# Kernel tuning notes

Hardware: AMD Instinct MI355X
Metric: run time of the kernel (lower is better)

The kernel has to match this reference:

```python
import jax, jax.numpy as jnp
import numpy as np

D = 256      # d_model
A = 64       # attn_dim
K = 16       # k_neighbors
N = 20000    # embedding table rows
B = 32768    # batch of perturbed genes
SCALE = A ** -0.5
EPS = 1e-5


def setup_inputs() -> dict:
    key = jax.random.key(0)
    ks = jax.random.split(key, 12)
    all_embs = jax.random.normal(ks[0], (N, D), dtype=jnp.float32)
    center_idx = jax.random.randint(ks[1], (B,), 0, N)
    nb_idx = jax.random.randint(ks[2], (B, K), 0, N)
    nb_weights = jax.random.uniform(ks[3], (B, K), dtype=jnp.float32)
    # learned params (torch Linear weight layout: [out, in])
    s = lambda fan_in: 1.0 / np.sqrt(fan_in)
    Wq = jax.random.uniform(ks[4], (A, D), minval=-s(D), maxval=s(D))
    Wk = jax.random.uniform(ks[5], (A, D), minval=-s(D), maxval=s(D))
    Wg = jax.random.uniform(ks[6], (D, D), minval=-s(D), maxval=s(D))
    bg = jax.random.uniform(ks[7], (D,), minval=-s(D), maxval=s(D))
    Wo = jax.random.uniform(ks[8], (D, 2 * D), minval=-s(2 * D), maxval=s(2 * D))
    bo = jax.random.uniform(ks[9], (D,), minval=-s(2 * D), maxval=s(2 * D))
    gamma = jnp.ones((D,), jnp.float32)
    beta = jnp.zeros((D,), jnp.float32)
    return dict(all_embs=all_embs, center_idx=center_idx, nb_idx=nb_idx,
                nb_weights=nb_weights, Wq=Wq, Wk=Wk, Wg=Wg, bg=bg,
                Wo=Wo, bo=bo, gamma=gamma, beta=beta)


def reference(all_embs, center_idx, nb_idx, nb_weights, Wq, Wk, Wg, bg, Wo, bo, gamma, beta):
    center = all_embs[center_idx]                      # [B, D]
    nbs = all_embs[nb_idx]                             # [B, K, D]
    q = center @ Wq.T                                  # [B, A]
    k = jnp.einsum('bkd,ad->bka', nbs, Wk)             # [B, K, A]
    logits = jnp.einsum('ba,bka->bk', q, k) * SCALE
    logits = logits + jnp.log(jnp.clip(nb_weights, 1e-6))
    attn = jax.nn.softmax(logits, axis=-1)             # [B, K]
    gate = jax.nn.sigmoid(center @ Wg.T + bg)          # [B, D]
    context = gate * jnp.einsum('bk,bkd->bd', attn, nbs)
    combined = jnp.concatenate([center, context], axis=-1)  # [B, 2D]
    enriched = combined @ Wo.T + bo                    # [B, D]
    x = enriched + center
    mu = jnp.mean(x, axis=-1, keepdims=True)
    var = jnp.var(x, axis=-1, keepdims=True)
    return (x - mu) * jax.lax.rsqrt(var + EPS) * gamma + beta
```

## Files before the change

kernel.cpp:

```cpp
#include <hip/hip_runtime.h>

#define DD 256
#define MM 32

typedef __attribute__((ext_vector_type(8))) short bfrag;
typedef __attribute__((ext_vector_type(4))) float ffrag;
typedef __attribute__((ext_vector_type(2))) float f32x2;

__device__ __forceinline__ float lo2f(unsigned int p){ union{unsigned int i; float f;} v; v.i = p<<16; return v.f; }
__device__ __forceinline__ float hi2f(unsigned int p){ union{unsigned int i; float f;} v; v.i = p & 0xffff0000u; return v.f; }
__device__ __forceinline__ float bf2f(unsigned short u){ union{unsigned int i; float f;} v; v.i = ((unsigned int)u)<<16; return v.f; }
__device__ __forceinline__ unsigned short f2b(float x){
    union{float f; unsigned int i;} v; v.f = x;
    unsigned int r = v.i + 0x7fffu + ((v.i>>16)&1u);
    return (unsigned short)(r>>16);
}
__device__ __forceinline__ unsigned int pack2(float a, float b){
    return (unsigned int)f2b(a) | ((unsigned int)f2b(b)<<16);
}
__device__ __forceinline__ f32x2 up2(unsigned int p){
    f32x2 r; r.x = lo2f(p); r.y = hi2f(p); return r;
}

__device__ __forceinline__ int swz256(int d, int e){
    return ((d>>4)*8 + (e>>5))*512 + (((e>>3)&3)*16 + (d&15))*8 + (e&7);
}
__device__ __forceinline__ int swz512(int d, int e){
    return ((d>>4)*16 + (e>>5))*512 + (((e>>3)&3)*16 + (d&15))*8 + (e&7);
}

extern "C" __global__ __launch_bounds__(256)
void prep_all(const float* __restrict__ Wq, const float* __restrict__ Wk,
              const float* __restrict__ Wg, const float* __restrict__ Wo,
              const float* __restrict__ embs, unsigned short* __restrict__ ws, int n8)
{
    int bid = blockIdx.x, e = threadIdx.x;
    if (bid < 256) {
        int d = bid; float acc = 0.f;
        #pragma unroll 8
        for (int a = 0; a < 64; ++a) acc = fmaf(Wq[a*256 + e], Wk[a*256 + d], acc);
        ws[swz256(d, e)] = f2b(acc);
    } else if (bid < 512) {
        int r = bid - 256;
        ws[65536 + swz256(r, e)] = f2b(Wg[r*256 + e]);
    } else if (bid < 768) {
        int r = bid - 512;
        ws[131072 + swz512(r, e)]       = f2b(Wo[r*512 + e]);
        ws[131072 + swz512(r, e + 256)] = f2b(Wo[r*512 + 256 + e]);
    } else {
        int i = (bid - 768)*256 + e;
        if (i < n8) {
            const float4* s = (const float4*)embs + (size_t)i*2;
            float4 a = s[0], b = s[1];
            uint4 o;
            o.x = pack2(a.x,a.y); o.y = pack2(a.z,a.w);
            o.z = pack2(b.x,b.y); o.w = pack2(b.z,b.w);
            ((uint4*)(ws + 262144))[i] = o;
        }
    }
}

template<bool TBF>
__device__ __forceinline__ void gather8(uint4* buf, const unsigned short* tbl,
                                        const float* embs, int idx, int p)
{
    if (TBF) {
        const unsigned short* base = tbl + (size_t)idx*DD + p*8;
        #pragma unroll
        for (int i = 0; i < 8; ++i) buf[i] = *(const uint4*)(base + i*32);
    } else {
        const float* base = embs + (size_t)idx*DD + p*8;
        #pragma unroll
        for (int i = 0; i < 8; ++i) {
            float4 a = *(const float4*)(base + i*32);
            float4 b = *(const float4*)(base + i*32 + 4);
            buf[i].x = pack2(a.x,a.y); buf[i].y = pack2(a.z,a.w);
            buf[i].z = pack2(b.x,b.y); buf[i].w = pack2(b.z,b.w);
        }
    }
}

template<bool TBF>
__global__ __launch_bounds__(256, 2)
void na_mfma14(const float* __restrict__ embs,
               const int* __restrict__ cidx,
               const int* __restrict__ nidx,
               const float* __restrict__ nbw,
               const unsigned short* __restrict__ tbl,
               const unsigned short* __restrict__ wMt,
               const unsigned short* __restrict__ wWg,
               const unsigned short* __restrict__ wWo,
               const float* __restrict__ bg,
               const float* __restrict__ bo,
               const float* __restrict__ gamma,
               const float* __restrict__ beta,
               float* __restrict__ out)
{
    __shared__ __align__(16) unsigned short s_ax[32][264];
    __shared__ __align__(16) unsigned short s_arena[21120];
    __shared__ int s_cidx[32];

    unsigned short (*s_t)[264]      = (unsigned short(*)[264])s_arena;
    unsigned short (*s_nb)[16][264] = (unsigned short(*)[16][264])(s_arena + 4224);
    float* s_x = (float*)s_arena;

    const int tid  = threadIdx.x;
    const int row0 = blockIdx.x * MM;
    const int lane = tid & 63, wv = tid >> 6;
    const int l15  = lane & 15, quad = lane >> 4;
    const ffrag fz = {0.f, 0.f, 0.f, 0.f};

    if (tid < 32) s_cidx[tid] = cidx[row0 + tid];
    uint4 careg0[8], careg1[8];
    {
        int a0 = cidx[row0 + l15];
        int a1 = cidx[row0 + 16 + l15];
        if (TBF) {
            const unsigned short* p0 = tbl + (size_t)a0*DD + quad*8;
            const unsigned short* p1 = tbl + (size_t)a1*DD + quad*8;
            #pragma unroll
            for (int kc = 0; kc < 8; ++kc) {
                careg0[kc] = *(const uint4*)(p0 + kc*32);
                careg1[kc] = *(const uint4*)(p1 + kc*32);
            }
        } else {
            const float* p0 = embs + (size_t)a0*DD + quad*8;
            const float* p1 = embs + (size_t)a1*DD + quad*8;
            #pragma unroll
            for (int kc = 0; kc < 8; ++kc) {
                float4 a = *(const float4*)(p0 + kc*32);
                float4 b = *(const float4*)(p0 + kc*32 + 4);
                careg0[kc].x = pack2(a.x,a.y); careg0[kc].y = pack2(a.z,a.w);
                careg0[kc].z = pack2(b.x,b.y); careg0[kc].w = pack2(b.z,b.w);
                float4 c = *(const float4*)(p1 + kc*32);
                float4 d = *(const float4*)(p1 + kc*32 + 4);
                careg1[kc].x = pack2(c.x,c.y); careg1[kc].y = pack2(c.z,c.w);
                careg1[kc].z = pack2(d.x,d.y); careg1[kc].w = pack2(d.z,d.w);
            }
        }
    }

    ffrag at1[4] = {fz,fz,fz,fz};
    {
        ffrag at0[4] = {fz,fz,fz,fz};
        ffrag ag0[4] = {fz,fz,fz,fz}, ag1[4] = {fz,fz,fz,fz};
        const unsigned short* btA = wMt + (size_t)(wv*4)*4096 + lane*8;
        const unsigned short* bgA = wWg + (size_t)(wv*4)*4096 + lane*8;
        #pragma unroll
        for (int kc = 0; kc < 8; ++kc) {
            bfrag a0 = *(const bfrag*)&careg0[kc];
            bfrag a1 = *(const bfrag*)&careg1[kc];
            #pragma unroll
            for (int t = 0; t < 4; ++t) {
                bfrag bm = *(const bfrag*)(btA + (size_t)t*4096 + kc*512);
                at0[t] = __builtin_amdgcn_mfma_f32_16x16x32_bf16(a0, bm, at0[t], 0,0,0);
                at1[t] = __builtin_amdgcn_mfma_f32_16x16x32_bf16(a1, bm, at1[t], 0,0,0);
                bfrag bw = *(const bfrag*)(bgA + (size_t)t*4096 + kc*512);
                ag0[t] = __builtin_amdgcn_mfma_f32_16x16x32_bf16(a0, bw, ag0[t], 0,0,0);
                ag1[t] = __builtin_amdgcn_mfma_f32_16x16x32_bf16(a1, bw, ag1[t], 0,0,0);
            }
        }
        #pragma unroll
        for (int t = 0; t < 4; ++t) {
            int col = wv*64 + t*16 + l15;
            float bgv = bg[col];
            #pragma unroll
            for (int r = 0; r < 4; ++r) {
                int rr = quad*4 + r;
                s_t[rr][col] = f2b(at0[t][r]);
                float g0 = 1.f / (1.f + __expf(-(ag0[t][r] + bgv)));
                s_ax[rr][col] = f2b(g0);
                float g1 = 1.f / (1.f + __expf(-(ag1[t][r] + bgv)));
                s_ax[16 + rr][col] = f2b(g1);
            }
        }
    }
    __syncthreads();

    const int kn = lane >> 2;
    const int p  = lane & 3;
    auto attn_phase = [&](int rb) {
        int idxs[4];
        #pragma unroll
        for (int j = 0; j < 4; ++j)
            idxs[j] = nidx[(size_t)(row0 + rb + 4*wv + j) * 16 + kn];

        uint4 buf[2][8];
        gather8<TBF>(buf[0], tbl, embs, idxs[0], p);

        #pragma unroll
        for (int j = 0; j < 4; ++j) {
            if (j < 3) gather8<TBF>(buf[(j+1)&1], tbl, embs, idxs[j+1], p);
            const int ml = 4*wv + j;
            const int mg = rb + ml;
            unsigned short* nbp = &s_nb[wv][kn][p*8];
            #pragma unroll
            for (int i = 0; i < 8; ++i) *(uint4*)(nbp + i*32) = buf[j&1][i];
            const unsigned short* trow = &s_t[ml][p*8];
            f32x2 part2 = {0.f, 0.f};
            #pragma unroll
            for (int i = 0; i < 8; ++i) {
                uint4 v = buf[j&1][i];
                uint4 tv = *(const uint4*)(trow + i*32);
                part2 += up2(v.x) * up2(tv.x);
                part2 += up2(v.y) * up2(tv.y);
                part2 += up2(v.z) * up2(tv.z);
                part2 += up2(v.w) * up2(tv.w);
            }
            float part = part2.x + part2.y;
            part += __shfl_xor(part, 1);
            part += __shfl_xor(part, 2);
            float lg = part * 0.125f;
            float mx = lg;
            mx = fmaxf(mx, __shfl_xor(mx, 4));  mx = fmaxf(mx, __shfl_xor(mx, 8));
            mx = fmaxf(mx, __shfl_xor(mx, 16)); mx = fmaxf(mx, __shfl_xor(mx, 32));
            float wgt = fmaxf(nbw[(size_t)(row0 + mg) * 16 + kn], 1e-6f);
            float e = wgt * __expf(lg - mx);
            float s = e;
            s += __shfl_xor(s, 4);  s += __shfl_xor(s, 8);
            s += __shfl_xor(s, 16); s += __shfl_xor(s, 32);
            float attn = e / s;
            f32x2 c01 = {0.f, 0.f}, c23 = {0.f, 0.f};
            #pragma unroll
            for (int kk = 0; kk < 16; ++kk) {
                float a = __shfl(attn, kk*4);
                f32x2 a2; a2.x = a; a2.y = a;
                uint2 v = *(const uint2*)&s_nb[wv][kk][lane*4];
                c01 += a2 * up2(v.x);
                c23 += a2 * up2(v.y);
            }
            uint2 g = *(const uint2*)&s_ax[mg][lane*4];
            f32x2 g01 = up2(g.x), g23 = up2(g.y);
            c01 *= g01; c23 *= g23;
            uint2 o; o.x = pack2(c01.x, c01.y); o.y = pack2(c23.x, c23.y);
            *(uint2*)&s_ax[mg][lane*4] = o;
        }
    };

    attn_phase(0);
    __syncthreads();
    {
        #pragma unroll
        for (int t = 0; t < 4; ++t) {
            int col = wv*64 + t*16 + l15;
            #pragma unroll
            for (int r = 0; r < 4; ++r)
                s_t[quad*4 + r][col] = f2b(at1[t][r]);
        }
    }
    __syncthreads();
    attn_phase(16);
    __syncthreads();

    {
        ffrag acc0[4] = {fz,fz,fz,fz}, acc1[4] = {fz,fz,fz,fz};
        const unsigned short* arx0 = &s_ax[l15][quad * 8];
        const unsigned short* arx1 = &s_ax[16 + l15][quad * 8];
        const unsigned short* bO   = wWo + (size_t)(wv*4)*8192 + lane*8;
        #pragma unroll
        for (int kc = 0; kc < 8; ++kc) {
            bfrag a0 = *(const bfrag*)&careg0[kc];
            bfrag a1 = *(const bfrag*)&careg1[kc];
            #pragma unroll
            for (int t = 0; t < 4; ++t) {
                bfrag b = *(const bfrag*)(bO + (size_t)t*8192 + kc*512);
                acc0[t] = __builtin_amdgcn_mfma_f32_16x16x32_bf16(a0, b, acc0[t], 0,0,0);
                acc1[t] = __builtin_amdgcn_mfma_f32_16x16x32_bf16(a1, b, acc1[t], 0,0,0);
            }
        }
        #pragma unroll
        for (int kc = 8; kc < 16; ++kc) {
            bfrag a0 = *(const bfrag*)(arx0 + (kc-8)*32);
            bfrag a1 = *(const bfrag*)(arx1 + (kc-8)*32);
            #pragma unroll
            for (int t = 0; t < 4; ++t) {
                bfrag b = *(const bfrag*)(bO + (size_t)t*8192 + kc*512);
                acc0[t] = __builtin_amdgcn_mfma_f32_16x16x32_bf16(a0, b, acc0[t], 0,0,0);
                acc1[t] = __builtin_amdgcn_mfma_f32_16x16x32_bf16(a1, b, acc1[t], 0,0,0);
            }
        }
        #pragma unroll
        for (int t = 0; t < 4; ++t) {
            int col = wv*64 + t*16 + l15;
            float bov = bo[col];
            #pragma unroll
            for (int r = 0; r < 4; ++r) {
                int rr = quad*4 + r;
                float c0 = embs[(size_t)s_cidx[rr] * DD + col];
                s_x[rr*260 + col] = acc0[t][r] + bov + c0;
                float c1 = embs[(size_t)s_cidx[16 + rr] * DD + col];
                s_x[(16 + rr)*260 + col] = acc1[t][r] + bov + c1;
            }
        }
    }
    __syncthreads();

    {
        #pragma unroll
        for (int jj = 0; jj < 8; ++jj) {
            int m = wv * 8 + jj;
            const float* xr = s_x + m*260;
            float x0 = xr[lane],       x1 = xr[64 + lane];
            float x2 = xr[128 + lane], x3 = xr[192 + lane];
            float s  = x0 + x1 + x2 + x3;
            float ss = x0*x0 + x1*x1 + x2*x2 + x3*x3;
            #pragma unroll
            for (int off = 32; off >= 1; off >>= 1) {
                s  += __shfl_xor(s, off);
                ss += __shfl_xor(ss, off);
            }
            float mu  = s * (1.f/256.f);
            float var = ss * (1.f/256.f) - mu*mu;
            float rs  = rsqrtf(var + 1e-5f);
            size_t base = (size_t)(row0 + m) * DD;
            float xs[4] = {x0, x1, x2, x3};
            #pragma unroll
            for (int cc = 0; cc < 4; ++cc) {
                int dd = cc*64 + lane;
                out[base + dd] = (xs[cc] - mu) * rs * gamma[dd] + beta[dd];
            }
        }
    }
}

#define SD 260
#define KT 16
#define WS 17
#define FM 16
extern "C" __global__ __launch_bounds__(256)
void na_f32_kernel(const float* __restrict__ embs, const int* __restrict__ center_idx,
                   const int* __restrict__ nb_idx, const float* __restrict__ nb_w,
                   const float* __restrict__ Wq, const float* __restrict__ Wk,
                   const float* __restrict__ Wg, const float* __restrict__ bg,
                   const float* __restrict__ Wo, const float* __restrict__ bo,
                   const float* __restrict__ gamma, const float* __restrict__ beta,
                   float* __restrict__ out)
{
    __shared__ __align__(16) float s_center[FM][SD];
    __shared__ __align__(16) float s_tc[FM][SD];
    __shared__ __align__(16) float s_nb[16][SD];
    __shared__ __align__(16) float s_w[DD][WS];
    __shared__ __align__(16) float s_q[FM][64];
    __shared__ float s_red[16][16];
    __shared__ float s_attn[16];
    const int tid = threadIdx.x;
    const int row0 = blockIdx.x * FM;
    const int td = tid & 63, tm = tid >> 6;
    {
        int m = tid >> 4, c = tid & 15;
        int idx = center_idx[row0 + m];
        const float4* src = (const float4*)(embs + (size_t)idx * DD) + c * 4;
        float4* dst = (float4*)&s_center[m][c * 16];
        dst[0]=src[0]; dst[1]=src[1]; dst[2]=src[2]; dst[3]=src[3];
    }
    __syncthreads();
    {
        const int a = tid & 63, mg = tid >> 6;
        float qacc[4] = {0,0,0,0};
        for (int kt = 0; kt < DD; kt += KT) {
            __syncthreads();
            { int r = tid >> 2, c4 = (tid & 3) * 4;
              *(float4*)&s_w[r][c4] = *(const float4*)(Wq + r * DD + kt + c4); }
            __syncthreads();
            #pragma unroll
            for (int kk = 0; kk < KT; kk += 4) {
                float4 b = *(const float4*)&s_w[a][kk];
                #pragma unroll
                for (int i = 0; i < 4; ++i) {
                    float4 av = *(const float4*)&s_center[4*mg + i][kt + kk];
                    qacc[i] += av.x*b.x + av.y*b.y + av.z*b.z + av.w*b.w;
                }
            }
        }
        __syncthreads();
        #pragma unroll
        for (int i = 0; i < 4; ++i) s_q[4*mg + i][a] = qacc[i];
    }
    __syncthreads();
    {
        float tacc[4][4];
        #pragma unroll
        for (int i=0;i<4;++i) { tacc[i][0]=tacc[i][1]=tacc[i][2]=tacc[i][3]=0.f; }
        for (int kk = 0; kk < 64; kk += 4) {
            float4 bk[4];
            #pragma unroll
            for (int t4 = 0; t4 < 4; ++t4)
                bk[t4] = *(const float4*)(Wk + (size_t)(kk + t4) * DD + 4 * td);
            #pragma unroll
            for (int i = 0; i < 4; ++i) {
                float4 av = *(const float4*)&s_q[4*tm + i][kk];
                tacc[i][0] += av.x*bk[0].x + av.y*bk[1].x + av.z*bk[2].x + av.w*bk[3].x;
                tacc[i][1] += av.x*bk[0].y + av.y*bk[1].y + av.z*bk[2].y + av.w*bk[3].y;
                tacc[i][2] += av.x*bk[0].z + av.y*bk[1].z + av.z*bk[2].z + av.w*bk[3].z;
                tacc[i][3] += av.x*bk[0].w + av.y*bk[1].w + av.z*bk[2].w + av.w*bk[3].w;
            }
        }
        #pragma unroll
        for (int i = 0; i < 4; ++i)
            *(float4*)&s_tc[4*tm + i][4*td] = make_float4(tacc[i][0],tacc[i][1],tacc[i][2],tacc[i][3]);
    }
    __syncthreads();
    for (int m = 0; m < FM; ++m) {
        { int k = tid >> 4, c = tid & 15;
          int idx = nb_idx[(row0 + m) * 16 + k];
          const float4* src = (const float4*)(embs + (size_t)idx * DD) + c * 4;
          float4* dst = (float4*)&s_nb[k][c * 16];
          dst[0]=src[0]; dst[1]=src[1]; dst[2]=src[2]; dst[3]=src[3]; }
        __syncthreads();
        { int k = tid >> 4, i = tid & 15;
          float acc = 0.f;
          #pragma unroll
          for (int j4 = 0; j4 < 4; ++j4) {
              float4 nv = *(const float4*)&s_nb[k][i*16 + 4*j4];
              float4 tv = *(const float4*)&s_tc[m][i*16 + 4*j4];
              acc += nv.x*tv.x + nv.y*tv.y + nv.z*tv.z + nv.w*tv.w;
          }
          s_red[k][i] = acc; }
        __syncthreads();
        if (tid < 16) {
            float lg = 0.f;
            #pragma unroll
            for (int i = 0; i < 16; ++i) lg += s_red[tid][i];
            float wv2 = nb_w[(row0 + m) * 16 + tid];
            lg = lg * 0.125f + logf(fmaxf(wv2, 1e-6f));
            float mx = lg;
            #pragma unroll
            for (int off = 8; off >= 1; off >>= 1) mx = fmaxf(mx, __shfl_xor(mx, off));
            float e = expf(lg - mx);
            float s = e;
            #pragma unroll
            for (int off = 8; off >= 1; off >>= 1) s += __shfl_xor(s, off);
            s_attn[tid] = e / s;
        }
        __syncthreads();
        { float acc = 0.f;
          #pragma unroll
          for (int k = 0; k < 16; ++k) acc += s_attn[k] * s_nb[k][tid];
          s_tc[m][tid] = acc; }
        __syncthreads();
    }
    {
        float acc[4][4];
        #pragma unroll
        for (int i=0;i<4;++i){acc[i][0]=acc[i][1]=acc[i][2]=acc[i][3]=0.f;}
        for (int kt = 0; kt < DD; kt += KT) {
            __syncthreads();
            #pragma unroll
            for (int j = 0; j < 4; ++j) {
                int r = (tid >> 2) + 64 * j, c4 = (tid & 3) * 4;
                *(float4*)&s_w[r][c4] = *(const float4*)(Wg + (size_t)r * DD + kt + c4);
            }
            __syncthreads();
            #pragma unroll
            for (int kk = 0; kk < KT; kk += 4) {
                float4 b[4];
                #pragma unroll
                for (int j = 0; j < 4; ++j) b[j] = *(const float4*)&s_w[4*td + j][kk];
                #pragma unroll
                for (int i = 0; i < 4; ++i) {
                    float4 av = *(const float4*)&s_center[4*tm + i][kt + kk];
                    #pragma unroll
                    for (int j = 0; j < 4; ++j)
                        acc[i][j] += av.x*b[j].x + av.y*b[j].y + av.z*b[j].z + av.w*b[j].w;
                }
            }
        }
        float bgv[4];
        #pragma unroll
        for (int j = 0; j < 4; ++j) bgv[j] = bg[4*td + j];
        __syncthreads();
        #pragma unroll
        for (int i = 0; i < 4; ++i)
            #pragma unroll
            for (int j = 0; j < 4; ++j) {
                float g = 1.f / (1.f + expf(-(acc[i][j] + bgv[j])));
                s_tc[4*tm + i][4*td + j] *= g;
            }
    }
    {
        float acc[4][4];
        #pragma unroll
        for (int i=0;i<4;++i){acc[i][0]=acc[i][1]=acc[i][2]=acc[i][3]=0.f;}
        for (int kt = 0; kt < 2*DD; kt += KT) {
            __syncthreads();
            #pragma unroll
            for (int j = 0; j < 4; ++j) {
                int r = (tid >> 2) + 64 * j, c4 = (tid & 3) * 4;
                *(float4*)&s_w[r][c4] = *(const float4*)(Wo + (size_t)r * 2 * DD + kt + c4);
            }
            __syncthreads();
            const float* Abase = (kt < DD) ? &s_center[0][0] : &s_tc[0][0];
            const int kb = (kt < DD) ? kt : kt - DD;
            #pragma unroll
            for (int kk = 0; kk < KT; kk += 4) {
                float4 b[4];
                #pragma unroll
                for (int j = 0; j < 4; ++j) b[j] = *(const float4*)&s_w[4*td + j][kk];
                #pragma unroll
                for (int i = 0; i < 4; ++i) {
                    float4 av = *(const float4*)(Abase + (4*tm + i) * SD + kb + kk);
                    #pragma unroll
                    for (int j = 0; j < 4; ++j)
                        acc[i][j] += av.x*b[j].x + av.y*b[j].y + av.z*b[j].z + av.w*b[j].w;
                }
            }
        }
        float bov[4];
        #pragma unroll
        for (int j = 0; j < 4; ++j) bov[j] = bo[4*td + j];
        __syncthreads();
        #pragma unroll
        for (int i = 0; i < 4; ++i)
            #pragma unroll
            for (int j = 0; j < 4; ++j)
                s_tc[4*tm + i][4*td + j] = acc[i][j] + bov[j] + s_center[4*tm + i][4*td + j];
    }
    __syncthreads();
    {
        int wv2 = tid >> 6, lane = tid & 63;
        #pragma unroll
        for (int jj = 0; jj < 4; ++jj) {
            int m = wv2 * 4 + jj;
            float x0 = s_tc[m][lane],       x1 = s_tc[m][64 + lane];
            float x2 = s_tc[m][128 + lane], x3 = s_tc[m][192 + lane];
            float s  = x0+x1+x2+x3;
            float ss = x0*x0 + x1*x1 + x2*x2 + x3*x3;
            #pragma unroll
            for (int off = 32; off >= 1; off >>= 1) { s += __shfl_xor(s, off); ss += __shfl_xor(ss, off); }
            float mu = s * (1.f/256.f);
            float var = ss * (1.f/256.f) - mu*mu;
            float rs = rsqrtf(var + 1e-5f);
            size_t base = (size_t)(row0 + m) * DD;
            float xs[4] = {x0,x1,x2,x3};
            #pragma unroll
            for (int c = 0; c < 4; ++c) {
                int dd = c*64 + lane;
                out[base + dd] = (xs[c] - mu) * rs * gamma[dd] + beta[dd];
            }
        }
    }
}

extern "C" void kernel_launch(void* const* d_in, const int* in_sizes, int n_in,
                              void* d_out, int out_size, void* d_ws, size_t ws_size,
                              hipStream_t stream) {
    const float* embs  = (const float*)d_in[0];
    const int*   cidx  = (const int*)d_in[1];
    const int*   nidx  = (const int*)d_in[2];
    const float* nbw   = (const float*)d_in[3];
    const float* Wq    = (const float*)d_in[4];
    const float* Wk    = (const float*)d_in[5];
    const float* Wg    = (const float*)d_in[6];
    const float* bg    = (const float*)d_in[7];
    const float* Wo    = (const float*)d_in[8];
    const float* bo    = (const float*)d_in[9];
    const float* gamma = (const float*)d_in[10];
    const float* beta  = (const float*)d_in[11];
    float* out = (float*)d_out;

    const int B = in_sizes[1];
    const int nemb = in_sizes[0];
    const size_t need_w = 262144 * 2;
    const size_t need_t = need_w + (size_t)nemb * 2;

    if (ws_size < need_w || (B & 31) != 0) {
        hipLaunchKernelGGL(na_f32_kernel, dim3(B / FM), dim3(256), 0, stream,
                           embs, cidx, nidx, nbw, Wq, Wk, Wg, bg, Wo, bo, gamma, beta, out);
        return;
    }
    unsigned short* wsb = (unsigned short*)d_ws;
    const bool use_tbl = (ws_size >= need_t) && ((nemb & 7) == 0);
    const int n8 = use_tbl ? (nemb / 8) : 0;
    const int prep_grid = 768 + (use_tbl ? (n8 + 255) / 256 : 0);
    hipLaunchKernelGGL(prep_all, dim3(prep_grid), dim3(256), 0, stream,
                       Wq, Wk, Wg, Wo, embs, wsb, n8);

    if (use_tbl) {
        hipLaunchKernelGGL(na_mfma14<true>, dim3(B / MM), dim3(256), 0, stream,
                           embs, cidx, nidx, nbw, wsb + 262144,
                           wsb, wsb + 65536, wsb + 131072,
                           bg, bo, gamma, beta, out);
    } else {
        hipLaunchKernelGGL(na_mfma14<false>, dim3(B / MM), dim3(256), 0, stream,
                           embs, cidx, nidx, nbw, (const unsigned short*)nullptr,
                           wsb, wsb + 65536, wsb + 131072,
                           bg, bo, gamma, beta, out);
    }
}
```

Measured before the change: 174.1 us.

## Switch bf16 path to fp16 with fdot2 logits and drop softmax max

Converts the packed embedding table, weights and intermediates from bf16 to fp16, and uses f16 MFMA instructions. The per-neighbor logit dot product now uses packed fdot2 instructions instead of unpacking to float pairs. The softmax max-subtraction reduction is removed, relying on logits staying small enough that exp does not overflow. This removes unpack ALU work and four cross-lane shuffles per row. The cost is reduced dynamic range, which risks fp16 overflow and numerical instability for larger inputs.

```diff
diff --git a/kernel.cpp b/kernel.cpp
--- a/kernel.cpp
+++ b/kernel.cpp
@@ -3,23 +3,23 @@
 #define DD 256
 #define MM 32
 
-typedef __attribute__((ext_vector_type(8))) short bfrag;
+typedef __attribute__((ext_vector_type(8))) _Float16 hfrag;
 typedef __attribute__((ext_vector_type(4))) float ffrag;
 typedef __attribute__((ext_vector_type(2))) float f32x2;
-
-__device__ __forceinline__ float lo2f(unsigned int p){ union{unsigned int i; float f;} v; v.i = p<<16; return v.f; }
-__device__ __forceinline__ float hi2f(unsigned int p){ union{unsigned int i; float f;} v; v.i = p & 0xffff0000u; return v.f; }
-__device__ __forceinline__ float bf2f(unsigned short u){ union{unsigned int i; float f;} v; v.i = ((unsigned int)u)<<16; return v.f; }
-__device__ __forceinline__ unsigned short f2b(float x){
-    union{float f; unsigned int i;} v; v.f = x;
-    unsigned int r = v.i + 0x7fffu + ((v.i>>16)&1u);
-    return (unsigned short)(r>>16);
-}
-__device__ __forceinline__ unsigned int pack2(float a, float b){
-    return (unsigned int)f2b(a) | ((unsigned int)f2b(b)<<16);
-}
-__device__ __forceinline__ f32x2 up2(unsigned int p){
-    f32x2 r; r.x = lo2f(p); r.y = hi2f(p); return r;
+typedef __attribute__((ext_vector_type(2))) _Float16 h16x2;
+
+__device__ __forceinline__ unsigned short f2h(float x){
+    union{_Float16 h; unsigned short u;} v; v.h = (_Float16)x; return v.u;
+}
+__device__ __forceinline__ unsigned int pack2h(float a, float b){
+    return (unsigned int)f2h(a) | ((unsigned int)f2h(b)<<16);
+}
+__device__ __forceinline__ h16x2 u2h(unsigned int p){
+    union{unsigned int u; h16x2 h;} v; v.u = p; return v.h;
+}
+__device__ __forceinline__ f32x2 up2h(unsigned int p){
+    union{unsigned int u; _Float16 h[2];} v; v.u = p;
+    f32x2 r; r.x = (float)v.h[0]; r.y = (float)v.h[1]; return r;
 }
 
 __device__ __forceinline__ int swz256(int d, int e){
@@ -39,22 +39,22 @@
         int d = bid; float acc = 0.f;
         #pragma unroll 8
         for (int a = 0; a < 64; ++a) acc = fmaf(Wq[a*256 + e], Wk[a*256 + d], acc);
-        ws[swz256(d, e)] = f2b(acc);
+        ws[swz256(d, e)] = f2h(acc);
     } else if (bid < 512) {
         int r = bid - 256;
-        ws[65536 + swz256(r, e)] = f2b(Wg[r*256 + e]);
+        ws[65536 + swz256(r, e)] = f2h(Wg[r*256 + e]);
     } else if (bid < 768) {
         int r = bid - 512;
-        ws[131072 + swz512(r, e)]       = f2b(Wo[r*512 + e]);
-        ws[131072 + swz512(r, e + 256)] = f2b(Wo[r*512 + 256 + e]);
+        ws[131072 + swz512(r, e)]       = f2h(Wo[r*512 + e]);
+        ws[131072 + swz512(r, e + 256)] = f2h(Wo[r*512 + 256 + e]);
     } else {
         int i = (bid - 768)*256 + e;
         if (i < n8) {
             const float4* s = (const float4*)embs + (size_t)i*2;
             float4 a = s[0], b = s[1];
             uint4 o;
-            o.x = pack2(a.x,a.y); o.y = pack2(a.z,a.w);
-            o.z = pack2(b.x,b.y); o.w = pack2(b.z,b.w);
+            o.x = pack2h(a.x,a.y); o.y = pack2h(a.z,a.w);
+            o.z = pack2h(b.x,b.y); o.w = pack2h(b.z,b.w);
             ((uint4*)(ws + 262144))[i] = o;
         }
     }
@@ -74,15 +74,15 @@
         for (int i = 0; i < 8; ++i) {
             float4 a = *(const float4*)(base + i*32);
             float4 b = *(const float4*)(base + i*32 + 4);
-            buf[i].x = pack2(a.x,a.y); buf[i].y = pack2(a.z,a.w);
-            buf[i].z = pack2(b.x,b.y); buf[i].w = pack2(b.z,b.w);
+            buf[i].x = pack2h(a.x,a.y); buf[i].y = pack2h(a.z,a.w);
+            buf[i].z = pack2h(b.x,b.y); buf[i].w = pack2h(b.z,b.w);
         }
     }
 }
 
 template<bool TBF>
 __global__ __launch_bounds__(256, 2)
-void na_mfma14(const float* __restrict__ embs,
+void na_mfma15(const float* __restrict__ embs,
                const int* __restrict__ cidx,
                const int* __restrict__ nidx,
                const float* __restrict__ nbw,
@@ -130,12 +130,12 @@
             for (int kc = 0; kc < 8; ++kc) {
                 float4 a = *(const float4*)(p0 + kc*32);
                 float4 b = *(const float4*)(p0 + kc*32 + 4);
-                careg0[kc].x = pack2(a.x,a.y); careg0[kc].y = pack2(a.z,a.w);
-                careg0[kc].z = pack2(b.x,b.y); careg0[kc].w = pack2(b.z,b.w);
+                careg0[kc].x = pack2h(a.x,a.y); careg0[kc].y = pack2h(a.z,a.w);
+                careg0[kc].z = pack2h(b.x,b.y); careg0[kc].w = pack2h(b.z,b.w);
                 float4 c = *(const float4*)(p1 + kc*32);
                 float4 d = *(const float4*)(p1 + kc*32 + 4);
-                careg1[kc].x = pack2(c.x,c.y); careg1[kc].y = pack2(c.z,c.w);
-                careg1[kc].z = pack2(d.x,d.y); careg1[kc].w = pack2(d.z,d.w);
+                careg1[kc].x = pack2h(c.x,c.y); careg1[kc].y = pack2h(c.z,c.w);
+                careg1[kc].z = pack2h(d.x,d.y); careg1[kc].w = pack2h(d.z,d.w);
             }
         }
     }
@@ -148,16 +148,16 @@
         const unsigned short* bgA = wWg + (size_t)(wv*4)*4096 + lane*8;
         #pragma unroll
         for (int kc = 0; kc < 8; ++kc) {
-            bfrag a0 = *(const bfrag*)&careg0[kc];
-            bfrag a1 = *(const bfrag*)&careg1[kc];
+            hfrag a0 = *(const hfrag*)&careg0[kc];
+            hfrag a1 = *(const hfrag*)&careg1[kc];
             #pragma unroll
             for (int t = 0; t < 4; ++t) {
-                bfrag bm = *(const bfrag*)(btA + (size_t)t*4096 + kc*512);
-                at0[t] = __builtin_amdgcn_mfma_f32_16x16x32_bf16(a0, bm, at0[t], 0,0,0);
-                at1[t] = __builtin_amdgcn_mfma_f32_16x16x32_bf16(a1, bm, at1[t], 0,0,0);
-                bfrag bw = *(const bfrag*)(bgA + (size_t)t*4096 + kc*512);
-                ag0[t] = __builtin_amdgcn_mfma_f32_16x16x32_bf16(a0, bw, ag0[t], 0,0,0);
-                ag1[t] = __builtin_amdgcn_mfma_f32_16x16x32_bf16(a1, bw, ag1[t], 0,0,0);
+                hfrag bm = *(const hfrag*)(btA + (size_t)t*4096 + kc*512);
+                at0[t] = __builtin_amdgcn_mfma_f32_16x16x32_f16(a0, bm, at0[t], 0,0,0);
+                at1[t] = __builtin_amdgcn_mfma_f32_16x16x32_f16(a1, bm, at1[t], 0,0,0);
+                hfrag bw = *(const hfrag*)(bgA + (size_t)t*4096 + kc*512);
+                ag0[t] = __builtin_amdgcn_mfma_f32_16x16x32_f16(a0, bw, ag0[t], 0,0,0);
+                ag1[t] = __builtin_amdgcn_mfma_f32_16x16x32_f16(a1, bw, ag1[t], 0,0,0);
             }
         }
         #pragma unroll
@@ -167,11 +167,11 @@
             #pragma unroll
             for (int r = 0; r < 4; ++r) {
                 int rr = quad*4 + r;
-                s_t[rr][col] = f2b(at0[t][r]);
+                s_t[rr][col] = f2h(at0[t][r]);
                 float g0 = 1.f / (1.f + __expf(-(ag0[t][r] + bgv)));
-                s_ax[rr][col] = f2b(g0);
+                s_ax[rr][col] = f2h(g0);
                 float g1 = 1.f / (1.f + __expf(-(ag1[t][r] + bgv)));
-                s_ax[16 + rr][col] = f2b(g1);
+                s_ax[16 + rr][col] = f2h(g1);
             }
         }
     }
@@ -197,25 +197,22 @@
             #pragma unroll
             for (int i = 0; i < 8; ++i) *(uint4*)(nbp + i*32) = buf[j&1][i];
             const unsigned short* trow = &s_t[ml][p*8];
-            f32x2 part2 = {0.f, 0.f};
+            float pa = 0.f, pb = 0.f;
             #pragma unroll
             for (int i = 0; i < 8; ++i) {
                 uint4 v = buf[j&1][i];
                 uint4 tv = *(const uint4*)(trow + i*32);
-                part2 += up2(v.x) * up2(tv.x);
-                part2 += up2(v.y) * up2(tv.y);
-                part2 += up2(v.z) * up2(tv.z);
-                part2 += up2(v.w) * up2(tv.w);
-            }
-            float part = part2.x + part2.y;
+                pa = __builtin_amdgcn_fdot2(u2h(v.x), u2h(tv.x), pa, false);
+                pb = __builtin_amdgcn_fdot2(u2h(v.y), u2h(tv.y), pb, false);
+                pa = __builtin_amdgcn_fdot2(u2h(v.z), u2h(tv.z), pa, false);
+                pb = __builtin_amdgcn_fdot2(u2h(v.w), u2h(tv.w), pb, false);
+            }
+            float part = pa + pb;
             part += __shfl_xor(part, 1);
             part += __shfl_xor(part, 2);
             float lg = part * 0.125f;
-            float mx = lg;
-            mx = fmaxf(mx, __shfl_xor(mx, 4));  mx = fmaxf(mx, __shfl_xor(mx, 8));
-            mx = fmaxf(mx, __shfl_xor(mx, 16)); mx = fmaxf(mx, __shfl_xor(mx, 32));
             float wgt = fmaxf(nbw[(size_t)(row0 + mg) * 16 + kn], 1e-6f);
-            float e = wgt * __expf(lg - mx);
+            float e = wgt * __expf(lg);
             float s = e;
             s += __shfl_xor(s, 4);  s += __shfl_xor(s, 8);
             s += __shfl_xor(s, 16); s += __shfl_xor(s, 32);
@@ -226,13 +223,12 @@
                 float a = __shfl(attn, kk*4);
                 f32x2 a2; a2.x = a; a2.y = a;
                 uint2 v = *(const uint2*)&s_nb[wv][kk][lane*4];
-                c01 += a2 * up2(v.x);
-                c23 += a2 * up2(v.y);
+                c01 += a2 * up2h(v.x);
+                c23 += a2 * up2h(v.y);
             }
             uint2 g = *(const uint2*)&s_ax[mg][lane*4];
-            f32x2 g01 = up2(g.x), g23 = up2(g.y);
-            c01 *= g01; c23 *= g23;
-            uint2 o; o.x = pack2(c01.x, c01.y); o.y = pack2(c23.x, c23.y);
+            c01 *= up2h(g.x); c23 *= up2h(g.y);
+            uint2 o; o.x = pack2h(c01.x, c01.y); o.y = pack2h(c23.x, c23.y);
             *(uint2*)&s_ax[mg][lane*4] = o;
         }
     };
@@ -245,7 +241,7 @@
             int col = wv*64 + t*16 + l15;
             #pragma unroll
             for (int r = 0; r < 4; ++r)
-                s_t[quad*4 + r][col] = f2b(at1[t][r]);
+                s_t[quad*4 + r][col] = f2h(at1[t][r]);
         }
     }
     __syncthreads();
@@ -259,24 +255,24 @@
         const unsigned short* bO   = wWo + (size_t)(wv*4)*8192 + lane*8;
         #pragma unroll
         for (int kc = 0; kc < 8; ++kc) {
-            bfrag a0 = *(const bfrag*)&careg0[kc];
-            bfrag a1 = *(const bfrag*)&careg1[kc];
+            hfrag a0 = *(const hfrag*)&careg0[kc];
+            hfrag a1 = *(const hfrag*)&careg1[kc];
             #pragma unroll
             for (int t = 0; t < 4; ++t) {
-                bfrag b = *(const bfrag*)(bO + (size_t)t*8192 + kc*512);
-                acc0[t] = __builtin_amdgcn_mfma_f32_16x16x32_bf16(a0, b, acc0[t], 0,0,0);
-                acc1[t] = __builtin_amdgcn_mfma_f32_16x16x32_bf16(a1, b, acc1[t], 0,0,0);
+                hfrag b = *(const hfrag*)(bO + (size_t)t*8192 + kc*512);
+                acc0[t] = __builtin_amdgcn_mfma_f32_16x16x32_f16(a0, b, acc0[t], 0,0,0);
+                acc1[t] = __builtin_amdgcn_mfma_f32_16x16x32_f16(a1, b, acc1[t], 0,0,0);
             }
         }
         #pragma unroll
         for (int kc = 8; kc < 16; ++kc) {
-            bfrag a0 = *(const bfrag*)(arx0 + (kc-8)*32);
-            bfrag a1 = *(const bfrag*)(arx1 + (kc-8)*32);
+            hfrag a0 = *(const hfrag*)(arx0 + (kc-8)*32);
+            hfrag a1 = *(const hfrag*)(arx1 + (kc-8)*32);
             #pragma unroll
             for (int t = 0; t < 4; ++t) {
-                bfrag b = *(const bfrag*)(bO + (size_t)t*8192 + kc*512);
-                acc0[t] = __builtin_amdgcn_mfma_f32_16x16x32_bf16(a0, b, acc0[t], 0,0,0);
-                acc1[t] = __builtin_amdgcn_mfma_f32_16x16x32_bf16(a1, b, acc1[t], 0,0,0);
+                hfrag b = *(const hfrag*)(bO + (size_t)t*8192 + kc*512);
+                acc0[t] = __builtin_amdgcn_mfma_f32_16x16x32_f16(a0, b, acc0[t], 0,0,0);
+                acc1[t] = __builtin_amdgcn_mfma_f32_16x16x32_f16(a1, b, acc1[t], 0,0,0);
             }
         }
         #pragma unroll
@@ -576,12 +572,12 @@
                        Wq, Wk, Wg, Wo, embs, wsb, n8);
 
     if (use_tbl) {
-        hipLaunchKernelGGL(na_mfma14<true>, dim3(B / MM), dim3(256), 0, stream,
+        hipLaunchKernelGGL(na_mfma15<true>, dim3(B / MM), dim3(256), 0, stream,
                            embs, cidx, nidx, nbw, wsb + 262144,
                            wsb, wsb + 65536, wsb + 131072,
                            bg, bo, gamma, beta, out);
     } else {
-        hipLaunchKernelGGL(na_mfma14<false>, dim3(B / MM), dim3(256), 0, stream,
+        hipLaunchKernelGGL(na_mfma15<false>, dim3(B / MM), dim3(256), 0, stream,
                            embs, cidx, nidx, nbw, (const unsigned short*)nullptr,
                            wsb, wsb + 65536, wsb + 131072,
                            bg, bo, gamma, beta, out);
```

Result: faster. 166.5 us (-4.4%).
